# Performance work log

Hardware: AMD Instinct MI355X
Metric: run time of the kernel (lower is better)

## Reference

```python
import jax, jax.numpy as jnp
import numpy as np

B, N, HN, HE, H = 8, 128, 256, 128, 8
DH = HN // H
P = N * (N - 1) // 2


def _ln(x, g, b, eps=1e-5):
    m = jnp.mean(x, axis=-1, keepdims=True)
    v = jnp.mean((x - m) ** 2, axis=-1, keepdims=True)
    return (x - m) * jax.lax.rsqrt(v + eps) * g + b


def setup_inputs() -> dict:
    key = jax.random.key(0)
    ks = jax.random.split(key, 16)
    i1, i2 = np.triu_indices(N, k=1)  # all unordered pairs, P = N(N-1)/2
    s = lambda fan: 1.0 / np.sqrt(fan)
    return {
        "node_feat": jax.random.normal(ks[0], (B, N, HN), jnp.float32),
        "edge_feat": jax.random.normal(ks[1], (B, P, HE), jnp.float32),
        "x_idx1": jnp.asarray(i1, jnp.int32),
        "x_idx2": jnp.asarray(i2, jnp.int32),
        "mask_valid": jax.random.bernoulli(ks[2], 0.9, (B, P)).astype(jnp.float32),
        "Wqkv": jax.random.normal(ks[3], (HN, 3 * HN), jnp.float32) * s(HN),
        "bqkv": jnp.zeros((3 * HN,), jnp.float32),
        "Wev": jax.random.normal(ks[4], (HE, HN), jnp.float32) * s(HE),
        "bev": jnp.zeros((HN,), jnp.float32),
        "Wea": jax.random.normal(ks[5], (HE, H), jnp.float32) * s(HE),
        "bea": jnp.zeros((H,), jnp.float32),
        "Wo": jax.random.normal(ks[6], (2 * HN, HN), jnp.float32) * s(2 * HN),
        "bo": jnp.zeros((HN,), jnp.float32),
        "Wsk": jax.random.normal(ks[7], (HN, 2 * HN), jnp.float32) * s(HN),
        "bsk": jnp.zeros((2 * HN,), jnp.float32),
        "gn": jnp.ones((HN,), jnp.float32),
        "bn": jnp.zeros((HN,), jnp.float32),
        "ge": jnp.ones((HE,), jnp.float32),
        "be": jnp.zeros((HE,), jnp.float32),
    }


def reference(node_feat, edge_feat, x_idx1, x_idx2, mask_valid,
              Wqkv, bqkv, Wev, bev, Wea, bea, Wo, bo, Wsk, bsk,
              gn, bn, ge, be):
    n_in = _ln(node_feat, gn, bn)                      # [B,N,HN]
    e_in = _ln(edge_feat, ge, be)                      # [B,P,HE]
    q, k, v = jnp.split(n_in @ Wqkv + bqkv, 3, axis=-1)
    to_h = lambda t: t.reshape(B, -1, H, DH).transpose(0, 2, 1, 3)
    q, k, v = to_h(q), to_h(k), to_h(v)                # [B,H,N,DH]
    e_val = to_h(e_in @ Wev + bev)                     # [B,H,P,DH]
    e_adj = (e_in @ Wea + bea).transpose(0, 2, 1)      # [B,H,P]

    scale = DH ** -0.5
    logits = jnp.einsum('bhqd,bhkd->bhqk', q, k) * scale  # [B,H,N,N]
    # per-pair logits; torch stacks [qk, edge_adj] then sums -> just add
    l_node1 = logits[:, :, x_idx1, x_idx2] + e_adj     # node i1 attends to i2
    l_node2 = logits[:, :, x_idx2, x_idx1] + e_adj     # node i2 attends to i1
    v_node1 = e_val + v[:, :, x_idx2]                  # value node i1 receives
    v_node2 = e_val + v[:, :, x_idx1]

    # group the 2P directed edges by destination node (= torch cat+sort+reshape)
    cat_idx = jnp.concatenate([x_idx1, x_idx2])        # [2P]
    order = jnp.argsort(cat_idx)                       # stable sort
    gl = jnp.concatenate([l_node1, l_node2], axis=2)[:, :, order].reshape(B, H, N, N - 1)
    gv = jnp.concatenate([v_node1, v_node2], axis=2)[:, :, order].reshape(B, H, N, N - 1, DH)
    gm = jnp.concatenate([mask_valid, mask_valid], axis=1)[:, order].reshape(B, N, N - 1)[:, None]  # [B,1,N,N-1]

    gl = jnp.where(gm == 0.0, -9e15, gl)
    probs = jax.nn.softmax(gl, axis=3)
    probs = probs * jnp.any(gm != 0.0, axis=3, keepdims=True).astype(probs.dtype)
    attn = jnp.einsum('bhnk,bhnkd->bhnd', probs, gv)   # [B,H,N,DH]
    attn = attn.transpose(0, 2, 1, 3).reshape(B, N, HN)

    comb = jax.nn.gelu(jnp.concatenate([n_in, attn], axis=-1) @ Wo + bo, approximate=False)
    val, gate = jnp.split(comb @ Wsk + bsk, 2, axis=-1)
    g = jax.nn.sigmoid(gate)
    return node_feat * (1.0 - g) + val * g
```

## Files before the change

kernel.cpp:

```cpp
#include <hip/hip_runtime.h>
#include <hip/hip_bf16.h>
#include <math.h>

#define BB 8
#define NN 128
#define HN 256
#define HE 128
#define NH 8
#define DH 32
#define PP 8128
#define BP (BB*PP)

typedef __hip_bfloat16 bf16;
typedef __hip_bfloat162 bf162;
typedef __attribute__((ext_vector_type(8))) short bf16x8;
typedef __attribute__((ext_vector_type(4))) float f32x4;

__device__ __forceinline__ float bf2f(bf16 x){ return __bfloat162float(x); }
__device__ __forceinline__ float bfraw2f(short u){
  return __uint_as_float(((unsigned)(unsigned short)u) << 16);
}

__device__ __forceinline__ float wave_sum(float v){
  #pragma unroll
  for (int off=32; off>=1; off>>=1) v += __shfl_xor(v, off, 64);
  return v;
}
__device__ __forceinline__ float wave_max(float v){
  #pragma unroll
  for (int off=32; off>=1; off>>=1) v = fmaxf(v, __shfl_xor(v, off, 64));
  return v;
}
__device__ __forceinline__ float g16_sum(float v){
  #pragma unroll
  for (int off=8; off>=1; off>>=1) v += __shfl_xor(v, off, 16);
  return v;
}

__device__ __forceinline__ int pair_idx(int a, int c){
  int i = a < c ? a : c;
  int j = a < c ? c : a;
  return ((i*(255 - i))>>1) + (j - i - 1);
}

#define C_NODE 0LL
#define C_MASK 262144LL
#define C_WQKV 327168LL
#define C_BQKV 523776LL
#define C_WEV  524544LL
#define C_BEV  557312LL
#define C_WEA  557568LL
#define C_BEA  558592LL
#define C_WO   558600LL
#define C_BO   689672LL
#define C_WSK  689928LL
#define C_BSK  821000LL
#define C_GN   821512LL
#define C_BN   821768LL
#define C_GE   822024LL
#define C_BE   822152LL
#define IOFF   822400LL
#define TOT8   102785
#define CONVBLKS 402
#define I_NIN  0LL
#define I_Q    262144LL
#define I_K    524288LL
#define I_V    786432LL
#define I_ATTN 1048576LL
#define I_COMB 1310720LL
#define I_EA2  1572864LL
#define I_XG   2093056LL
#define I_EVAL 6254592LL
#define I_WT   14577664LL
#define I_WOB  14594048LL
#define I_WSKB 14659584LL
#define I_FLG  14725120LL

struct SrcPtrs { const void* p[16]; };

__global__ __launch_bounds__(256) void k_convert(SrcPtrs sp, float* __restrict__ dst,
                                                 int* __restrict__ flags,
                                                 const unsigned short* __restrict__ nodeRaw,
                                                 const void* __restrict__ rawWev,
                                                 bf16* __restrict__ Wt,
                                                 const void* __restrict__ rawWo,
                                                 const void* __restrict__ rawWsk,
                                                 bf16* __restrict__ WoB,
                                                 bf16* __restrict__ WskB)
{
  __shared__ int sbad;
  if (threadIdx.x == 0) sbad = 0;
  __syncthreads();
  {
    int bad = 0;
    for (int i = threadIdx.x; i < 1024; i += 256){
      unsigned e = (nodeRaw[i] >> 7) & 0xFFu;
      if (e >= 194u) bad = 1;
    }
    if (bad) sbad = 1;
  }
  __syncthreads();
  const int f32 = sbad;
  if (blockIdx.x == 0 && threadIdx.x == 0) flags[0] = f32;

  if (blockIdx.x >= CONVBLKS + 128){
    int o = (blockIdx.x - (CONVBLKS + 128))*256 + threadIdx.x;
    const void* src = (o < 16384) ? rawWo : rawWsk;
    bf16* dw = (o < 16384) ? WoB : WskB;
    int lo = (o < 16384) ? o : o - 16384;
    if (f32){
      const float4* s4 = (const float4*)src;
      float4 a0 = s4[2*lo], a1 = s4[2*lo+1];
      union { float4 f; bf16 h[8]; } cv;
      cv.h[0]=__float2bfloat16(a0.x); cv.h[1]=__float2bfloat16(a0.y);
      cv.h[2]=__float2bfloat16(a0.z); cv.h[3]=__float2bfloat16(a0.w);
      cv.h[4]=__float2bfloat16(a1.x); cv.h[5]=__float2bfloat16(a1.y);
      cv.h[6]=__float2bfloat16(a1.z); cv.h[7]=__float2bfloat16(a1.w);
      *reinterpret_cast<float4*>(dw + lo*8) = cv.f;
    } else {
      *reinterpret_cast<float4*>(dw + lo*8) = ((const float4*)src)[lo];
    }
    return;
  }

  if (blockIdx.x >= CONVBLKS){
    int idx = (blockIdx.x - CONVBLKS)*256 + threadIdx.x;
    float v = f32 ? ((const float*)rawWev)[idx]
                  : bfraw2f(((const short*)rawWev)[idx]);
    Wt[(idx & 255)*128 + (idx >> 8)] = __float2bfloat16(v);
    return;
  }

  int o = blockIdx.x*256 + threadIdx.x;
  if (o >= TOT8) return;
  const int cum[17] = {0,32768,40896,65472,65568,69664,69696,69824,69825,
                       86209,86241,102625,102689,102721,102753,102769,102785};
  int s = 0;
  #pragma unroll
  for (int i = 1; i <= 15; i++) if (o >= cum[i]) s = i;
  const int li = o - cum[s];
  float4 r0, r1;
  if (f32){
    const float4* src = (const float4*)sp.p[s];
    r0 = src[2*li]; r1 = src[2*li+1];
  } else {
    union { float4 f; unsigned short u[8]; } cv;
    cv.f = ((const float4*)sp.p[s])[li];
    r0.x = __uint_as_float((unsigned)cv.u[0] << 16);
    r0.y = __uint_as_float((unsigned)cv.u[1] << 16);
    r0.z = __uint_as_float((unsigned)cv.u[2] << 16);
    r0.w = __uint_as_float((unsigned)cv.u[3] << 16);
    r1.x = __uint_as_float((unsigned)cv.u[4] << 16);
    r1.y = __uint_as_float((unsigned)cv.u[5] << 16);
    r1.z = __uint_as_float((unsigned)cv.u[6] << 16);
    r1.w = __uint_as_float((unsigned)cv.u[7] << 16);
  }
  float4* d = (float4*)(dst + (long long)cum[s]*8);
  d[2*li]   = r0;
  d[2*li+1] = r1;
}

__global__ __launch_bounds__(256) void k1_node_ln_qkv(
    const float* __restrict__ cnode, const float* __restrict__ cWqkv,
    const float* __restrict__ cbqkv, const float* __restrict__ cgn, const float* __restrict__ cbn,
    float* __restrict__ nin_ws, float* __restrict__ q_ws, float* __restrict__ k_ws,
    float* __restrict__ v_ws)
{
  __shared__ float xln[4][HN];
  const int t = threadIdx.x, wv = t>>6, lane = t&63;
  const int cb = blockIdx.x % 3;
  const int g0 = (blockIdx.x / 3) * 4;
  {
    int g = g0 + wv;
    float x[4];
    #pragma unroll
    for (int i=0;i<4;i++) x[i] = cnode[g*HN + lane + 64*i];
    float s = x[0]+x[1]+x[2]+x[3];
    s = wave_sum(s);
    float m = s * (1.0f/HN);
    float q = 0.f;
    #pragma unroll
    for (int i=0;i<4;i++){ float d = x[i]-m; q += d*d; }
    q = wave_sum(q);
    float rstd = rsqrtf(fmaxf(q*(1.0f/HN), 0.f) + 1e-5f);
    #pragma unroll
    for (int i=0;i<4;i++){
      int c = lane + 64*i;
      float y = (x[i]-m)*rstd*cgn[c] + cbn[c];
      xln[wv][c] = y;
      if (cb == 0) nin_ws[g*HN + c] = y;
    }
  }
  __syncthreads();
  const int col = cb*256 + t;
  float acc[4];
  {
    float bb = cbqkv[col];
    #pragma unroll
    for (int r=0;r<4;r++) acc[r] = bb;
  }
  for (int k=0;k<HN;k+=4){
    float4 xv[4];
    #pragma unroll
    for (int r=0;r<4;r++) xv[r] = *reinterpret_cast<const float4*>(&xln[r][k]);
    #pragma unroll
    for (int kk=0;kk<4;kk++){
      float w = cWqkv[(k+kk)*768 + col];
      #pragma unroll
      for (int r=0;r<4;r++) acc[r] = fmaf((&xv[r].x)[kk], w, acc[r]);
    }
  }
  float* dstp = (cb == 0) ? q_ws : (cb == 1) ? k_ws : v_ws;
  const int h = t>>5, d = t&31;
  #pragma unroll
  for (int r=0;r<4;r++){
    int g = g0 + r;
    int b = g>>7, n = g&127;
    dstp[((b*NH + h)*NN + n)*DH + d] = acc[r];
  }
}

__global__ __launch_bounds__(256) void k2a_edge_ln(
    const void* __restrict__ edge_raw, const float* __restrict__ cWea,
    const float* __restrict__ cbea, const float* __restrict__ cge,
    const float* __restrict__ cbe, const float* __restrict__ cmask,
    bf16* __restrict__ xg, float* __restrict__ ea2, const int* __restrict__ flags)
{
  __shared__ float xlnS[16][136];
  __shared__ float part[128];
  const int t = threadIdx.x;
  const int R0 = blockIdx.x*16;
  const int b = R0 / PP;
  const int p0 = R0 - b*PP;
  const int f32 = flags[0];
  {
    int r = t>>4, sub = t&15;
    long base = (long)(R0 + r)*HE + sub*8;
    float x[8];
    if (f32){
      const float* cef = (const float*)edge_raw + base;
      float4 a0 = *reinterpret_cast<const float4*>(cef);
      float4 a1 = *reinterpret_cast<const float4*>(cef + 4);
      x[0]=a0.x; x[1]=a0.y; x[2]=a0.z; x[3]=a0.w;
      x[4]=a1.x; x[5]=a1.y; x[6]=a1.z; x[7]=a1.w;
    } else {
      union { float4 f; short u[8]; } cv;
      cv.f = *reinterpret_cast<const float4*>((const bf16*)edge_raw + base);
      #pragma unroll
      for (int i=0;i<8;i++) x[i] = bfraw2f(cv.u[i]);
    }
    float s = 0.f;
    #pragma unroll
    for (int i=0;i<8;i++) s += x[i];
    s = g16_sum(s);
    float m = s*(1.0f/HE);
    float q = 0.f;
    #pragma unroll
    for (int i=0;i<8;i++){ float dd = x[i]-m; q += dd*dd; }
    q = g16_sum(q);
    float rstd = rsqrtf(fmaxf(q*(1.0f/HE), 0.f) + 1e-5f);
    #pragma unroll
    for (int i=0;i<8;i++){
      int c = sub*8 + i;
      xlnS[r][c] = (x[i]-m)*rstd*cge[c] + cbe[c];
    }
  }
  __syncthreads();
  {
    int r = t>>4, c0 = (t&15)*8;
    union { float4 f; bf16 h[8]; } o;
    #pragma unroll
    for (int i=0;i<8;i++) o.h[i] = __float2bfloat16(xlnS[r][c0+i]);
    *reinterpret_cast<float4*>(xg + (long)(R0 + r)*HE + c0) = o.f;
  }
  {
    const int c = t & 7, r = (t>>3) & 15, half = t>>7;
    const int pid = r*8 + c;
    float s = half ? 0.0f : cbea[c];
    const int k0 = half*64;
    #pragma unroll 8
    for (int k=k0; k<k0+64; k++) s = fmaf(xlnS[r][k], cWea[k*NH + c], s);
    if (half){ part[pid] = s; }
    __syncthreads();
    if (!half){
      s += part[pid];
      int p = p0 + r;
      float mk = cmask[b*PP + p];
      ea2[(b*NH + c)*PP + p] = (mk != 0.0f) ? s : -9e15f;
    }
  }
}

__global__ __launch_bounds__(256) void k2b_mfma(
    const bf16* __restrict__ xg, const bf16* __restrict__ Wt,
    const float* __restrict__ cbev, bf16* __restrict__ e_val)
{
  __shared__ bf16 Xs[64][136];
  __shared__ bf16 Ws[64][136];
  const int t = threadIdx.x;
  const int rowblk = blockIdx.x >> 2;
  const int cb = blockIdx.x & 3;
  const int b = rowblk / 127;
  const int p0 = (rowblk - b*127) * 64;
  const int n0 = cb * 64;
  #pragma unroll
  for (int it = 0; it < 4; ++it){
    int idx = it*256 + t;
    int r = idx >> 4, seg = idx & 15;
    float4 xv = *reinterpret_cast<const float4*>(xg + (long)(b*PP + p0 + r)*HE + seg*8);
    *reinterpret_cast<float4*>(&Xs[r][seg*8]) = xv;
    float4 wv = *reinterpret_cast<const float4*>(Wt + (long)(n0 + r)*HE + seg*8);
    *reinterpret_cast<float4*>(&Ws[r][seg*8]) = wv;
  }
  __syncthreads();
  const int wv = t>>6, lane = t&63;
  const int fm = lane & 15, q = lane >> 4;
  f32x4 acc[4];
  #pragma unroll
  for (int ct=0; ct<4; ++ct){
    float bb = cbev[n0 + ct*16 + fm];
    acc[ct][0]=bb; acc[ct][1]=bb; acc[ct][2]=bb; acc[ct][3]=bb;
  }
  #pragma unroll
  for (int ks=0; ks<4; ++ks){
    bf16x8 A = *reinterpret_cast<const bf16x8*>(&Xs[wv*16 + fm][ks*32 + q*8]);
    #pragma unroll
    for (int ct=0; ct<4; ++ct){
      bf16x8 Bf = *reinterpret_cast<const bf16x8*>(&Ws[ct*16 + fm][ks*32 + q*8]);
      acc[ct] = __builtin_amdgcn_mfma_f32_16x16x32_bf16(A, Bf, acc[ct], 0, 0, 0);
    }
  }
  #pragma unroll
  for (int ct=0; ct<4; ++ct){
    int col = n0 + ct*16 + fm;
    int h = col >> 5, d = col & 31;
    #pragma unroll
    for (int reg=0; reg<4; ++reg){
      int p = p0 + wv*16 + q*4 + reg;
      e_val[((long)(b*NH + h)*PP + p)*DH + d] = __float2bfloat16(acc[ct][reg]);
    }
  }
}

__global__ __launch_bounds__(256) void k3_attn(
    const float* __restrict__ q_ws, const float* __restrict__ k_ws, const float* __restrict__ v_ws,
    const bf16* __restrict__ e_val, const float* __restrict__ ea2,
    float* __restrict__ attn)
{
  __shared__ float kT[DH][NN+1];
  __shared__ float vS[NN][DH+1];
  __shared__ float qS[8][DH];
  __shared__ float pbuf[4][NN];
  const int t = threadIdx.x, wv = t>>6, lane = t&63;
  const int s16 = blockIdx.x & 15, h = (blockIdx.x>>4)&7, b = blockIdx.x>>7;
  const int bh = b*NH + h;
  const int n0 = s16*8;
  const float* kb = k_ws + (long)bh*NN*DH;
  const float* vb = v_ws + (long)bh*NN*DH;
  const float* qb = q_ws + ((long)bh*NN + n0)*DH;
  for (int idx=t; idx<NN*DH; idx+=256){
    int m = idx>>5, d = idx&31;
    kT[d][m] = kb[idx];
    vS[m][d] = vb[idx];
  }
  if (t < 8*DH) reinterpret_cast<float*>(qS)[t] = qb[t];
  __syncthreads();
  const float scale = 0.17677669529663687f;
  const float* eab = ea2 + (long)bh*PP;
  const bf16* evp = e_val + (long)bh*PP*DH;
  for (int it=0; it<2; ++it){
    const int nn = it*4 + wv;
    const int n = n0 + nn;
    const int m1 = lane, m2 = lane + 64;
    float dot1 = 0.f, dot2 = 0.f;
    #pragma unroll
    for (int d=0; d<DH; d++){
      float qd = qS[nn][d];
      dot1 = fmaf(qd, kT[d][m1], dot1);
      dot2 = fmaf(qd, kT[d][m2], dot2);
    }
    const bool self1 = (m1 == n), self2 = (m2 == n);
    int pr1 = pair_idx(n, self1 ? (m1^1) : m1);
    int pr2 = pair_idx(n, self2 ? (m2^1) : m2);
    float ea1 = eab[pr1], ea2v = eab[pr2];
    float l1 = self1 ? -INFINITY : dot1*scale + ea1;
    float l2 = self2 ? -INFINITY : dot2*scale + ea2v;
    bool av = (!self1 && ea1 > -8.9e15f) || (!self2 && ea2v > -8.9e15f);
    float lm = wave_max(fmaxf(l1, l2));
    float e1 = __expf(l1 - lm), e2 = __expf(l2 - lm);
    float ssum = wave_sum(e1 + e2);
    int anyv = __any((int)av);
    float inv = anyv ? (1.0f/ssum) : 0.0f;
    pbuf[wv][m1] = e1*inv;
    pbuf[wv][m2] = e2*inv;
    const int msub = lane & 15, oct = lane >> 4;
    float acc[8];
    #pragma unroll
    for (int e=0;e<8;e++) acc[e] = 0.f;
    #pragma unroll
    for (int mm=0; mm<128; mm+=16){
      int m = mm + msub;
      int ms = (m==n) ? (m^1) : m;
      int pr = pair_idx(n, ms);
      bf16x8 ev8 = *reinterpret_cast<const bf16x8*>(evp + (long)pr*DH + oct*8);
      float pm = pbuf[wv][m];
      const float* vrow = &vS[m][oct*8];
      #pragma unroll
      for (int e=0;e<8;e++){
        acc[e] = fmaf(pm, vrow[e] + bfraw2f(ev8[e]), acc[e]);
      }
    }
    #pragma unroll
    for (int off=1; off<16; off<<=1){
      #pragma unroll
      for (int e=0;e<8;e++) acc[e] += __shfl_xor(acc[e], off, 64);
    }
    if (msub == 0){
      float* op = attn + ((long)b*NN + n)*HN + h*DH + oct*8;
      float4 o0 = {acc[0],acc[1],acc[2],acc[3]};
      float4 o1 = {acc[4],acc[5],acc[6],acc[7]};
      *reinterpret_cast<float4*>(op) = o0;
      *reinterpret_cast<float4*>(op+4) = o1;
    }
  }
}

__global__ __launch_bounds__(256) void k4_wo_gelu(
    const float* __restrict__ nin_ws, const float* __restrict__ attn,
    const bf16* __restrict__ WoB, const float* __restrict__ cbo,
    float* __restrict__ comb)
{
  __shared__ float xc[4][512];
  __shared__ float ps[3][4][64];
  const int t = threadIdx.x;
  const int g0 = (blockIdx.x >> 2) * 4;
  const int cq = blockIdx.x & 3;
  {
    int r = t>>6, c0 = (t&63)*8;
    const float* src = (c0 < 256) ? (nin_ws + (long)(g0+r)*HN + c0)
                                  : (attn + (long)(g0+r)*HN + (c0-256));
    float4 a0 = *reinterpret_cast<const float4*>(src);
    float4 a1 = *reinterpret_cast<const float4*>(src+4);
    *reinterpret_cast<float4*>(&xc[r][c0]) = a0;
    *reinterpret_cast<float4*>(&xc[r][c0+4]) = a1;
  }
  __syncthreads();
  const int cidx = t & 63, ks = t >> 6;
  const int col = cq*64 + cidx;
  float acc[4] = {0.f,0.f,0.f,0.f};
  const int k0 = ks*128;
  #pragma unroll 4
  for (int k=k0; k<k0+128; k++){
    float w = bf2f(WoB[k*HN + col]);
    #pragma unroll
    for (int r=0;r<4;r++) acc[r] = fmaf(xc[r][k], w, acc[r]);
  }
  if (ks){
    #pragma unroll
    for (int r=0;r<4;r++) ps[ks-1][r][cidx] = acc[r];
  }
  __syncthreads();
  if (!ks){
    float bb = cbo[col];
    #pragma unroll
    for (int r=0;r<4;r++){
      float x = acc[r] + bb + ps[0][r][cidx] + ps[1][r][cidx] + ps[2][r][cidx];
      comb[(long)(g0+r)*HN + col] = 0.5f*x*(1.0f + erff(x*0.7071067811865475f));
    }
  }
}

__global__ __launch_bounds__(256) void k5_sk_gate(
    const float* __restrict__ comb, const float* __restrict__ cnode,
    const bf16* __restrict__ WskB, const float* __restrict__ cbsk,
    void* __restrict__ out, const int* __restrict__ flags)
{
  __shared__ float xc[4][HN];
  __shared__ float psv[3][4][64];
  __shared__ float psg[3][4][64];
  const int t = threadIdx.x;
  const int g0 = (blockIdx.x >> 2) * 4;
  const int cq = blockIdx.x & 3;
  {
    int r = t>>6, c0 = (t&63)*4;
    *reinterpret_cast<float4*>(&xc[r][c0]) =
        *reinterpret_cast<const float4*>(comb + (long)(g0+r)*HN + c0);
  }
  __syncthreads();
  const int cidx = t & 63, ks = t >> 6;
  const int col = cq*64 + cidx;
  float av[4] = {0.f,0.f,0.f,0.f}, ag[4] = {0.f,0.f,0.f,0.f};
  const int k0 = ks*64;
  #pragma unroll 4
  for (int k=k0; k<k0+64; k++){
    float wv = bf2f(WskB[k*512 + col]);
    float wg = bf2f(WskB[k*512 + col + 256]);
    #pragma unroll
    for (int r=0;r<4;r++){
      float xr = xc[r][k];
      av[r] = fmaf(xr, wv, av[r]);
      ag[r] = fmaf(xr, wg, ag[r]);
    }
  }
  if (ks){
    #pragma unroll
    for (int r=0;r<4;r++){ psv[ks-1][r][cidx] = av[r]; psg[ks-1][r][cidx] = ag[r]; }
  }
  __syncthreads();
  if (!ks){
    const int f32 = flags[0];
    float bv = cbsk[col], bg = cbsk[col+256];
    #pragma unroll
    for (int r=0;r<4;r++){
      float v = av[r] + bv + psv[0][r][cidx] + psv[1][r][cidx] + psv[2][r][cidx];
      float g = ag[r] + bg + psg[0][r][cidx] + psg[1][r][cidx] + psg[2][r][cidx];
      float gg = 1.0f/(1.0f + __expf(-g));
      float nf = cnode[(long)(g0+r)*HN + col];
      float res = nf*(1.0f - gg) + v*gg;
      if (f32) ((float*)out)[(long)(g0+r)*HN + col] = res;
      else ((bf16*)out)[(long)(g0+r)*HN + col] = __float2bfloat16(res);
    }
  }
}

extern "C" void kernel_launch(void* const* d_in, const int* in_sizes, int n_inputs,
                              void* d_out, int out_size, void* d_ws, size_t ws_size,
                              hipStream_t stream)
{
  float* ws = (float*)d_ws;
  float* c_node = ws + C_NODE;
  float* c_mask = ws + C_MASK;
  float* c_Wqkv = ws + C_WQKV;
  float* c_bqkv = ws + C_BQKV;
  float* c_bev  = ws + C_BEV;
  float* c_Wea  = ws + C_WEA;
  float* c_bea  = ws + C_BEA;
  float* c_bo   = ws + C_BO;
  float* c_bsk  = ws + C_BSK;
  float* c_gn   = ws + C_GN;
  float* c_bn   = ws + C_BN;
  float* c_ge   = ws + C_GE;
  float* c_be   = ws + C_BE;
  float* base   = ws + IOFF;
  float* nin_ws  = base + I_NIN;
  float* q_ws    = base + I_Q;
  float* k_ws    = base + I_K;
  float* v_ws    = base + I_V;
  float* attn_ws = base + I_ATTN;
  float* comb_ws = base + I_COMB;
  float* ea2_ws  = base + I_EA2;
  bf16*  xg_ws   = (bf16*)(base + I_XG);
  bf16*  eval_ws = (bf16*)(base + I_EVAL);
  bf16*  wt_ws   = (bf16*)(base + I_WT);
  bf16*  wob_ws  = (bf16*)(base + I_WOB);
  bf16*  wskb_ws = (bf16*)(base + I_WSKB);
  int*   flags   = (int*)(base + I_FLG);

  SrcPtrs sp;
  sp.p[0]  = d_in[0];
  sp.p[1]  = d_in[4];
  sp.p[2]  = d_in[5];
  sp.p[3]  = d_in[6];
  sp.p[4]  = d_in[7];
  sp.p[5]  = d_in[8];
  sp.p[6]  = d_in[9];
  sp.p[7]  = d_in[10];
  sp.p[8]  = d_in[11];
  sp.p[9]  = d_in[12];
  sp.p[10] = d_in[13];
  sp.p[11] = d_in[14];
  sp.p[12] = d_in[15];
  sp.p[13] = d_in[16];
  sp.p[14] = d_in[17];
  sp.p[15] = d_in[18];

  k_convert<<<CONVBLKS + 256, 256, 0, stream>>>(sp, ws, flags,
                                                (const unsigned short*)d_in[0],
                                                d_in[7], wt_ws,
                                                d_in[11], d_in[13],
                                                wob_ws, wskb_ws);
  k1_node_ln_qkv<<<768, 256, 0, stream>>>(c_node, c_Wqkv, c_bqkv, c_gn, c_bn,
                                          nin_ws, q_ws, k_ws, v_ws);
  k2a_edge_ln<<<BP/16, 256, 0, stream>>>(d_in[1], c_Wea, c_bea, c_ge, c_be, c_mask,
                                         xg_ws, ea2_ws, flags);
  k2b_mfma<<<4064, 256, 0, stream>>>(xg_ws, wt_ws, c_bev, eval_ws);
  k3_attn<<<BB*NH*16, 256, 0, stream>>>(q_ws, k_ws, v_ws, eval_ws, ea2_ws, attn_ws);
  k4_wo_gelu<<<1024, 256, 0, stream>>>(nin_ws, attn_ws, wob_ws, c_bo, comb_ws);
  k5_sk_gate<<<1024, 256, 0, stream>>>(comb_ws, c_node, wskb_ws, c_bsk, d_out, flags);
}
```

Baseline: 199.5 us.

## Drop conversion kernel, read raw inputs directly and fuse node/edge LN kernels

Removes the separate format-conversion pre-pass and has every kernel read the raw input tensors directly. Each kernel re-detects the dtype from a sample of node_feat instead of reading a flag. The node LN+QKV kernel and the edge LN kernel are merged into one launch split by block index, and k2b now transposes the Wev tile itself while loading it into shared memory. This cuts one launch and the extra round trip through workspace, at the cost of a duplicated per-block dtype check and a strided, bank-conflicting shared-memory transpose in every k2b block.

```diff
diff --git a/kernel.cpp b/kernel.cpp
--- a/kernel.cpp
+++ b/kernel.cpp
@@ -12,11 +12,9 @@
 #define BP (BB*PP)
 
 typedef __hip_bfloat16 bf16;
-typedef __hip_bfloat162 bf162;
 typedef __attribute__((ext_vector_type(8))) short bf16x8;
 typedef __attribute__((ext_vector_type(4))) float f32x4;
 
-__device__ __forceinline__ float bf2f(bf16 x){ return __bfloat162float(x); }
 __device__ __forceinline__ float bfraw2f(short u){
   return __uint_as_float(((unsigned)(unsigned short)u) << 16);
 }
@@ -43,25 +41,35 @@
   return ((i*(255 - i))>>1) + (j - i - 1);
 }
 
-#define C_NODE 0LL
-#define C_MASK 262144LL
-#define C_WQKV 327168LL
-#define C_BQKV 523776LL
-#define C_WEV  524544LL
-#define C_BEV  557312LL
-#define C_WEA  557568LL
-#define C_BEA  558592LL
-#define C_WO   558600LL
-#define C_BO   689672LL
-#define C_WSK  689928LL
-#define C_BSK  821000LL
-#define C_GN   821512LL
-#define C_BN   821768LL
-#define C_GE   822024LL
-#define C_BE   822152LL
-#define IOFF   822400LL
-#define TOT8   102785
-#define CONVBLKS 402
+__device__ __forceinline__ int detect_f32(const unsigned short* __restrict__ nodeRaw){
+  __shared__ int sbad;
+  if (threadIdx.x == 0) sbad = 0;
+  __syncthreads();
+  int bad = 0;
+  for (int i = threadIdx.x; i < 1024; i += 256){
+    unsigned e = (nodeRaw[i] >> 7) & 0xFFu;
+    if (e >= 194u) bad = 1;
+  }
+  if (bad) sbad = 1;
+  __syncthreads();
+  return sbad;
+}
+
+__device__ __forceinline__ void load4raw(const void* raw, long off, int f32, float x[4]){
+  if (f32){
+    float4 v = *reinterpret_cast<const float4*>((const float*)raw + off);
+    x[0]=v.x; x[1]=v.y; x[2]=v.z; x[3]=v.w;
+  } else {
+    union { float2 f; short u[4]; } cv;
+    cv.f = *reinterpret_cast<const float2*>((const short*)raw + off);
+    #pragma unroll
+    for (int i=0;i<4;i++) x[i] = bfraw2f(cv.u[i]);
+  }
+}
+__device__ __forceinline__ float ldraw(const void* raw, long off, int f32){
+  return f32 ? ((const float*)raw)[off] : bfraw2f(((const short*)raw)[off]);
+}
+
 #define I_NIN  0LL
 #define I_Q    262144LL
 #define I_K    524288LL
@@ -71,232 +79,166 @@
 #define I_EA2  1572864LL
 #define I_XG   2093056LL
 #define I_EVAL 6254592LL
-#define I_WT   14577664LL
-#define I_WOB  14594048LL
-#define I_WSKB 14659584LL
-#define I_FLG  14725120LL
-
-struct SrcPtrs { const void* p[16]; };
-
-__global__ __launch_bounds__(256) void k_convert(SrcPtrs sp, float* __restrict__ dst,
-                                                 int* __restrict__ flags,
-                                                 const unsigned short* __restrict__ nodeRaw,
-                                                 const void* __restrict__ rawWev,
-                                                 bf16* __restrict__ Wt,
-                                                 const void* __restrict__ rawWo,
-                                                 const void* __restrict__ rawWsk,
-                                                 bf16* __restrict__ WoB,
-                                                 bf16* __restrict__ WskB)
-{
-  __shared__ int sbad;
-  if (threadIdx.x == 0) sbad = 0;
-  __syncthreads();
-  {
-    int bad = 0;
-    for (int i = threadIdx.x; i < 1024; i += 256){
-      unsigned e = (nodeRaw[i] >> 7) & 0xFFu;
-      if (e >= 194u) bad = 1;
-    }
-    if (bad) sbad = 1;
-  }
-  __syncthreads();
-  const int f32 = sbad;
-  if (blockIdx.x == 0 && threadIdx.x == 0) flags[0] = f32;
-
-  if (blockIdx.x >= CONVBLKS + 128){
-    int o = (blockIdx.x - (CONVBLKS + 128))*256 + threadIdx.x;
-    const void* src = (o < 16384) ? rawWo : rawWsk;
-    bf16* dw = (o < 16384) ? WoB : WskB;
-    int lo = (o < 16384) ? o : o - 16384;
-    if (f32){
-      const float4* s4 = (const float4*)src;
-      float4 a0 = s4[2*lo], a1 = s4[2*lo+1];
-      union { float4 f; bf16 h[8]; } cv;
-      cv.h[0]=__float2bfloat16(a0.x); cv.h[1]=__float2bfloat16(a0.y);
-      cv.h[2]=__float2bfloat16(a0.z); cv.h[3]=__float2bfloat16(a0.w);
-      cv.h[4]=__float2bfloat16(a1.x); cv.h[5]=__float2bfloat16(a1.y);
-      cv.h[6]=__float2bfloat16(a1.z); cv.h[7]=__float2bfloat16(a1.w);
-      *reinterpret_cast<float4*>(dw + lo*8) = cv.f;
-    } else {
-      *reinterpret_cast<float4*>(dw + lo*8) = ((const float4*)src)[lo];
-    }
-    return;
-  }
-
-  if (blockIdx.x >= CONVBLKS){
-    int idx = (blockIdx.x - CONVBLKS)*256 + threadIdx.x;
-    float v = f32 ? ((const float*)rawWev)[idx]
-                  : bfraw2f(((const short*)rawWev)[idx]);
-    Wt[(idx & 255)*128 + (idx >> 8)] = __float2bfloat16(v);
-    return;
-  }
-
-  int o = blockIdx.x*256 + threadIdx.x;
-  if (o >= TOT8) return;
-  const int cum[17] = {0,32768,40896,65472,65568,69664,69696,69824,69825,
-                       86209,86241,102625,102689,102721,102753,102769,102785};
-  int s = 0;
-  #pragma unroll
-  for (int i = 1; i <= 15; i++) if (o >= cum[i]) s = i;
-  const int li = o - cum[s];
-  float4 r0, r1;
-  if (f32){
-    const float4* src = (const float4*)sp.p[s];
-    r0 = src[2*li]; r1 = src[2*li+1];
-  } else {
-    union { float4 f; unsigned short u[8]; } cv;
-    cv.f = ((const float4*)sp.p[s])[li];
-    r0.x = __uint_as_float((unsigned)cv.u[0] << 16);
-    r0.y = __uint_as_float((unsigned)cv.u[1] << 16);
-    r0.z = __uint_as_float((unsigned)cv.u[2] << 16);
-    r0.w = __uint_as_float((unsigned)cv.u[3] << 16);
-    r1.x = __uint_as_float((unsigned)cv.u[4] << 16);
-    r1.y = __uint_as_float((unsigned)cv.u[5] << 16);
-    r1.z = __uint_as_float((unsigned)cv.u[6] << 16);
-    r1.w = __uint_as_float((unsigned)cv.u[7] << 16);
-  }
-  float4* d = (float4*)(dst + (long long)cum[s]*8);
-  d[2*li]   = r0;
-  d[2*li+1] = r1;
-}
-
-__global__ __launch_bounds__(256) void k1_node_ln_qkv(
-    const float* __restrict__ cnode, const float* __restrict__ cWqkv,
-    const float* __restrict__ cbqkv, const float* __restrict__ cgn, const float* __restrict__ cbn,
+
+__global__ __launch_bounds__(256) void kA_ln_qkv_edge(
+    const void* __restrict__ rawNode, const void* __restrict__ rawEdge,
+    const void* __restrict__ rawMask, const void* __restrict__ rawWqkv,
+    const void* __restrict__ rawBqkv, const void* __restrict__ rawWea,
+    const void* __restrict__ rawBea, const void* __restrict__ rawGn,
+    const void* __restrict__ rawBn, const void* __restrict__ rawGe,
+    const void* __restrict__ rawBe,
     float* __restrict__ nin_ws, float* __restrict__ q_ws, float* __restrict__ k_ws,
-    float* __restrict__ v_ws)
+    float* __restrict__ v_ws, bf16* __restrict__ xg, float* __restrict__ ea2)
 {
   __shared__ float xln[4][HN];
-  const int t = threadIdx.x, wv = t>>6, lane = t&63;
-  const int cb = blockIdx.x % 3;
-  const int g0 = (blockIdx.x / 3) * 4;
-  {
-    int g = g0 + wv;
-    float x[4];
-    #pragma unroll
-    for (int i=0;i<4;i++) x[i] = cnode[g*HN + lane + 64*i];
-    float s = x[0]+x[1]+x[2]+x[3];
-    s = wave_sum(s);
-    float m = s * (1.0f/HN);
-    float q = 0.f;
-    #pragma unroll
-    for (int i=0;i<4;i++){ float d = x[i]-m; q += d*d; }
-    q = wave_sum(q);
-    float rstd = rsqrtf(fmaxf(q*(1.0f/HN), 0.f) + 1e-5f);
-    #pragma unroll
-    for (int i=0;i<4;i++){
-      int c = lane + 64*i;
-      float y = (x[i]-m)*rstd*cgn[c] + cbn[c];
-      xln[wv][c] = y;
-      if (cb == 0) nin_ws[g*HN + c] = y;
-    }
-  }
-  __syncthreads();
-  const int col = cb*256 + t;
-  float acc[4];
-  {
-    float bb = cbqkv[col];
-    #pragma unroll
-    for (int r=0;r<4;r++) acc[r] = bb;
-  }
-  for (int k=0;k<HN;k+=4){
-    float4 xv[4];
-    #pragma unroll
-    for (int r=0;r<4;r++) xv[r] = *reinterpret_cast<const float4*>(&xln[r][k]);
-    #pragma unroll
-    for (int kk=0;kk<4;kk++){
-      float w = cWqkv[(k+kk)*768 + col];
-      #pragma unroll
-      for (int r=0;r<4;r++) acc[r] = fmaf((&xv[r].x)[kk], w, acc[r]);
-    }
-  }
-  float* dstp = (cb == 0) ? q_ws : (cb == 1) ? k_ws : v_ws;
-  const int h = t>>5, d = t&31;
-  #pragma unroll
-  for (int r=0;r<4;r++){
-    int g = g0 + r;
-    int b = g>>7, n = g&127;
-    dstp[((b*NH + h)*NN + n)*DH + d] = acc[r];
-  }
-}
-
-__global__ __launch_bounds__(256) void k2a_edge_ln(
-    const void* __restrict__ edge_raw, const float* __restrict__ cWea,
-    const float* __restrict__ cbea, const float* __restrict__ cge,
-    const float* __restrict__ cbe, const float* __restrict__ cmask,
-    bf16* __restrict__ xg, float* __restrict__ ea2, const int* __restrict__ flags)
-{
   __shared__ float xlnS[16][136];
   __shared__ float part[128];
+  const int f32 = detect_f32((const unsigned short*)rawNode);
   const int t = threadIdx.x;
-  const int R0 = blockIdx.x*16;
-  const int b = R0 / PP;
-  const int p0 = R0 - b*PP;
-  const int f32 = flags[0];
-  {
-    int r = t>>4, sub = t&15;
-    long base = (long)(R0 + r)*HE + sub*8;
-    float x[8];
-    if (f32){
-      const float* cef = (const float*)edge_raw + base;
-      float4 a0 = *reinterpret_cast<const float4*>(cef);
-      float4 a1 = *reinterpret_cast<const float4*>(cef + 4);
-      x[0]=a0.x; x[1]=a0.y; x[2]=a0.z; x[3]=a0.w;
-      x[4]=a1.x; x[5]=a1.y; x[6]=a1.z; x[7]=a1.w;
+
+  if (blockIdx.x < 768){
+    const int wv = t>>6, lane = t&63;
+    const int cb = blockIdx.x % 3;
+    const int g0 = (blockIdx.x / 3) * 4;
+    {
+      int g = g0 + wv;
+      float x[4], gn4[4], bn4[4];
+      load4raw(rawNode, (long)g*HN + lane*4, f32, x);
+      float s = x[0]+x[1]+x[2]+x[3];
+      s = wave_sum(s);
+      float m = s * (1.0f/HN);
+      float q = 0.f;
+      #pragma unroll
+      for (int i=0;i<4;i++){ float d = x[i]-m; q += d*d; }
+      q = wave_sum(q);
+      float rstd = rsqrtf(fmaxf(q*(1.0f/HN), 0.f) + 1e-5f);
+      load4raw(rawGn, lane*4, f32, gn4);
+      load4raw(rawBn, lane*4, f32, bn4);
+      float y4[4];
+      #pragma unroll
+      for (int i=0;i<4;i++){
+        y4[i] = (x[i]-m)*rstd*gn4[i] + bn4[i];
+        xln[wv][lane*4+i] = y4[i];
+      }
+      if (cb == 0){
+        float4 yo = {y4[0],y4[1],y4[2],y4[3]};
+        *reinterpret_cast<float4*>(nin_ws + (long)g*HN + lane*4) = yo;
+      }
+    }
+    __syncthreads();
+    const int col = cb*256 + t;
+    float acc[4];
+    {
+      float bb = ldraw(rawBqkv, col, f32);
+      #pragma unroll
+      for (int r=0;r<4;r++) acc[r] = bb;
+    }
+    if (!f32){
+      const short* W = (const short*)rawWqkv;
+      for (int k=0;k<HN;k+=4){
+        float4 xv[4];
+        #pragma unroll
+        for (int r=0;r<4;r++) xv[r] = *reinterpret_cast<const float4*>(&xln[r][k]);
+        #pragma unroll
+        for (int kk=0;kk<4;kk++){
+          float w = bfraw2f(W[(long)(k+kk)*768 + col]);
+          #pragma unroll
+          for (int r=0;r<4;r++) acc[r] = fmaf((&xv[r].x)[kk], w, acc[r]);
+        }
+      }
     } else {
-      union { float4 f; short u[8]; } cv;
-      cv.f = *reinterpret_cast<const float4*>((const bf16*)edge_raw + base);
-      #pragma unroll
-      for (int i=0;i<8;i++) x[i] = bfraw2f(cv.u[i]);
-    }
-    float s = 0.f;
-    #pragma unroll
-    for (int i=0;i<8;i++) s += x[i];
-    s = g16_sum(s);
-    float m = s*(1.0f/HE);
-    float q = 0.f;
-    #pragma unroll
-    for (int i=0;i<8;i++){ float dd = x[i]-m; q += dd*dd; }
-    q = g16_sum(q);
-    float rstd = rsqrtf(fmaxf(q*(1.0f/HE), 0.f) + 1e-5f);
-    #pragma unroll
-    for (int i=0;i<8;i++){
-      int c = sub*8 + i;
-      xlnS[r][c] = (x[i]-m)*rstd*cge[c] + cbe[c];
-    }
-  }
-  __syncthreads();
-  {
-    int r = t>>4, c0 = (t&15)*8;
-    union { float4 f; bf16 h[8]; } o;
-    #pragma unroll
-    for (int i=0;i<8;i++) o.h[i] = __float2bfloat16(xlnS[r][c0+i]);
-    *reinterpret_cast<float4*>(xg + (long)(R0 + r)*HE + c0) = o.f;
-  }
-  {
-    const int c = t & 7, r = (t>>3) & 15, half = t>>7;
-    const int pid = r*8 + c;
-    float s = half ? 0.0f : cbea[c];
-    const int k0 = half*64;
-    #pragma unroll 8
-    for (int k=k0; k<k0+64; k++) s = fmaf(xlnS[r][k], cWea[k*NH + c], s);
-    if (half){ part[pid] = s; }
+      const float* W = (const float*)rawWqkv;
+      for (int k=0;k<HN;k+=4){
+        float4 xv[4];
+        #pragma unroll
+        for (int r=0;r<4;r++) xv[r] = *reinterpret_cast<const float4*>(&xln[r][k]);
+        #pragma unroll
+        for (int kk=0;kk<4;kk++){
+          float w = W[(long)(k+kk)*768 + col];
+          #pragma unroll
+          for (int r=0;r<4;r++) acc[r] = fmaf((&xv[r].x)[kk], w, acc[r]);
+        }
+      }
+    }
+    float* dstp = (cb == 0) ? q_ws : (cb == 1) ? k_ws : v_ws;
+    const int h = t>>5, d = t&31;
+    #pragma unroll
+    for (int r=0;r<4;r++){
+      int g = g0 + r;
+      int b = g>>7, n = g&127;
+      dstp[((long)(b*NH + h)*NN + n)*DH + d] = acc[r];
+    }
+  } else {
+    const int R0 = (blockIdx.x - 768)*16;
+    const int b = R0 / PP;
+    const int p0 = R0 - b*PP;
+    {
+      int r = t>>4, sub = t&15;
+      long base = (long)(R0 + r)*HE + sub*8;
+      float x[8], ge8[8], be8[8];
+      load4raw(rawEdge, base, f32, x);
+      load4raw(rawEdge, base+4, f32, x+4);
+      load4raw(rawGe, sub*8, f32, ge8);
+      load4raw(rawGe, sub*8+4, f32, ge8+4);
+      load4raw(rawBe, sub*8, f32, be8);
+      load4raw(rawBe, sub*8+4, f32, be8+4);
+      float s = 0.f;
+      #pragma unroll
+      for (int i=0;i<8;i++) s += x[i];
+      s = g16_sum(s);
+      float m = s*(1.0f/HE);
+      float q = 0.f;
+      #pragma unroll
+      for (int i=0;i<8;i++){ float dd = x[i]-m; q += dd*dd; }
+      q = g16_sum(q);
+      float rstd = rsqrtf(fmaxf(q*(1.0f/HE), 0.f) + 1e-5f);
+      #pragma unroll
+      for (int i=0;i<8;i++){
+        xlnS[r][sub*8+i] = (x[i]-m)*rstd*ge8[i] + be8[i];
+      }
+    }
     __syncthreads();
-    if (!half){
-      s += part[pid];
-      int p = p0 + r;
-      float mk = cmask[b*PP + p];
-      ea2[(b*NH + c)*PP + p] = (mk != 0.0f) ? s : -9e15f;
+    {
+      int r = t>>4, c0 = (t&15)*8;
+      union { float4 f; bf16 h[8]; } o;
+      #pragma unroll
+      for (int i=0;i<8;i++) o.h[i] = __float2bfloat16(xlnS[r][c0+i]);
+      *reinterpret_cast<float4*>(xg + (long)(R0 + r)*HE + c0) = o.f;
+    }
+    {
+      const int c = t & 7, r = (t>>3) & 15, half = t>>7;
+      const int pid = r*8 + c;
+      float s = half ? 0.0f : ldraw(rawBea, c, f32);
+      const int k0 = half*64;
+      if (!f32){
+        const short* W = (const short*)rawWea;
+        #pragma unroll 8
+        for (int k=k0; k<k0+64; k++) s = fmaf(xlnS[r][k], bfraw2f(W[k*NH + c]), s);
+      } else {
+        const float* W = (const float*)rawWea;
+        #pragma unroll 8
+        for (int k=k0; k<k0+64; k++) s = fmaf(xlnS[r][k], W[k*NH + c], s);
+      }
+      if (half){ part[pid] = s; }
+      __syncthreads();
+      if (!half){
+        s += part[pid];
+        int p = p0 + r;
+        float mk = ldraw(rawMask, (long)b*PP + p, f32);
+        ea2[(long)(b*NH + c)*PP + p] = (mk != 0.0f) ? s : -9e15f;
+      }
     }
   }
 }
 
 __global__ __launch_bounds__(256) void k2b_mfma(
-    const bf16* __restrict__ xg, const bf16* __restrict__ Wt,
-    const float* __restrict__ cbev, bf16* __restrict__ e_val)
+    const void* __restrict__ rawNode,
+    const bf16* __restrict__ xg, const void* __restrict__ rawWev,
+    const void* __restrict__ rawBev, bf16* __restrict__ e_val)
 {
   __shared__ bf16 Xs[64][136];
   __shared__ bf16 Ws[64][136];
+  const int f32 = detect_f32((const unsigned short*)rawNode);
   const int t = threadIdx.x;
   const int rowblk = blockIdx.x >> 2;
   const int cb = blockIdx.x & 3;
@@ -309,8 +251,15 @@
     int r = idx >> 4, seg = idx & 15;
     float4 xv = *reinterpret_cast<const float4*>(xg + (long)(b*PP + p0 + r)*HE + seg*8);
     *reinterpret_cast<float4*>(&Xs[r][seg*8]) = xv;
-    float4 wv = *reinterpret_cast<const float4*>(Wt + (long)(n0 + r)*HE + seg*8);
-    *reinterpret_cast<float4*>(&Ws[r][seg*8]) = wv;
+  }
+  #pragma unroll
+  for (int it = 0; it < 8; ++it){
+    int r = it*16 + (t>>4);
+    int c0 = (t&15)*4;
+    float v[4];
+    load4raw(rawWev, (long)r*HN + n0 + c0, f32, v);
+    #pragma unroll
+    for (int j=0;j<4;j++) Ws[c0+j][r] = __float2bfloat16(v[j]);
   }
   __syncthreads();
   const int wv = t>>6, lane = t&63;
@@ -318,7 +267,7 @@
   f32x4 acc[4];
   #pragma unroll
   for (int ct=0; ct<4; ++ct){
-    float bb = cbev[n0 + ct*16 + fm];
+    float bb = ldraw(rawBev, n0 + ct*16 + fm, f32);
     acc[ct][0]=bb; acc[ct][1]=bb; acc[ct][2]=bb; acc[ct][3]=bb;
   }
   #pragma unroll
@@ -426,12 +375,14 @@
 }
 
 __global__ __launch_bounds__(256) void k4_wo_gelu(
+    const void* __restrict__ rawNode,
     const float* __restrict__ nin_ws, const float* __restrict__ attn,
-    const bf16* __restrict__ WoB, const float* __restrict__ cbo,
+    const void* __restrict__ rawWo, const void* __restrict__ rawBo,
     float* __restrict__ comb)
 {
   __shared__ float xc[4][512];
   __shared__ float ps[3][4][64];
+  const int f32 = detect_f32((const unsigned short*)rawNode);
   const int t = threadIdx.x;
   const int g0 = (blockIdx.x >> 2) * 4;
   const int cq = blockIdx.x & 3;
@@ -449,11 +400,22 @@
   const int col = cq*64 + cidx;
   float acc[4] = {0.f,0.f,0.f,0.f};
   const int k0 = ks*128;
-  #pragma unroll 4
-  for (int k=k0; k<k0+128; k++){
-    float w = bf2f(WoB[k*HN + col]);
-    #pragma unroll
-    for (int r=0;r<4;r++) acc[r] = fmaf(xc[r][k], w, acc[r]);
+  if (!f32){
+    const short* W = (const short*)rawWo;
+    #pragma unroll 4
+    for (int k=k0; k<k0+128; k++){
+      float w = bfraw2f(W[(long)k*HN + col]);
+      #pragma unroll
+      for (int r=0;r<4;r++) acc[r] = fmaf(xc[r][k], w, acc[r]);
+    }
+  } else {
+    const float* W = (const float*)rawWo;
+    #pragma unroll 4
+    for (int k=k0; k<k0+128; k++){
+      float w = W[(long)k*HN + col];
+      #pragma unroll
+      for (int r=0;r<4;r++) acc[r] = fmaf(xc[r][k], w, acc[r]);
+    }
   }
   if (ks){
     #pragma unroll
@@ -461,7 +423,7 @@
   }
   __syncthreads();
   if (!ks){
-    float bb = cbo[col];
+    float bb = ldraw(rawBo, col, f32);
     #pragma unroll
     for (int r=0;r<4;r++){
       float x = acc[r] + bb + ps[0][r][cidx] + ps[1][r][cidx] + ps[2][r][cidx];
@@ -471,13 +433,14 @@
 }
 
 __global__ __launch_bounds__(256) void k5_sk_gate(
-    const float* __restrict__ comb, const float* __restrict__ cnode,
-    const bf16* __restrict__ WskB, const float* __restrict__ cbsk,
-    void* __restrict__ out, const int* __restrict__ flags)
+    const void* __restrict__ rawNode,
+    const float* __restrict__ comb, const void* __restrict__ rawWsk,
+    const void* __restrict__ rawBsk, void* __restrict__ out)
 {
   __shared__ float xc[4][HN];
   __shared__ float psv[3][4][64];
   __shared__ float psg[3][4][64];
+  const int f32 = detect_f32((const unsigned short*)rawNode);
   const int t = threadIdx.x;
   const int g0 = (blockIdx.x >> 2) * 4;
   const int cq = blockIdx.x & 3;
@@ -491,15 +454,31 @@
   const int col = cq*64 + cidx;
   float av[4] = {0.f,0.f,0.f,0.f}, ag[4] = {0.f,0.f,0.f,0.f};
   const int k0 = ks*64;
-  #pragma unroll 4
-  for (int k=k0; k<k0+64; k++){
-    float wv = bf2f(WskB[k*512 + col]);
-    float wg = bf2f(WskB[k*512 + col + 256]);
-    #pragma unroll
-    for (int r=0;r<4;r++){
-      float xr = xc[r][k];
-      av[r] = fmaf(xr, wv, av[r]);
-      ag[r] = fmaf(xr, wg, ag[r]);
+  if (!f32){
+    const short* W = (const short*)rawWsk;
+    #pragma unroll 4
+    for (int k=k0; k<k0+64; k++){
+      float wv = bfraw2f(W[(long)k*512 + col]);
+      float wg = bfraw2f(W[(long)k*512 + col + 256]);
+      #pragma unroll
+      for (int r=0;r<4;r++){
+        float xr = xc[r][k];
+        av[r] = fmaf(xr, wv, av[r]);
+        ag[r] = fmaf(xr, wg, ag[r]);
+      }
+    }
+  } else {
+    const float* W = (const float*)rawWsk;
+    #pragma unroll 4
+    for (int k=k0; k<k0+64; k++){
+      float wv = W[(long)k*512 + col];
+      float wg = W[(long)k*512 + col + 256];
+      #pragma unroll
+      for (int r=0;r<4;r++){
+        float xr = xc[r][k];
+        av[r] = fmaf(xr, wv, av[r]);
+        ag[r] = fmaf(xr, wg, ag[r]);
+      }
     }
   }
   if (ks){
@@ -508,14 +487,13 @@
   }
   __syncthreads();
   if (!ks){
-    const int f32 = flags[0];
-    float bv = cbsk[col], bg = cbsk[col+256];
+    float bv = ldraw(rawBsk, col, f32), bg = ldraw(rawBsk, col+256, f32);
     #pragma unroll
     for (int r=0;r<4;r++){
       float v = av[r] + bv + psv[0][r][cidx] + psv[1][r][cidx] + psv[2][r][cidx];
       float g = ag[r] + bg + psg[0][r][cidx] + psg[1][r][cidx] + psg[2][r][cidx];
       float gg = 1.0f/(1.0f + __expf(-g));
-      float nf = cnode[(long)(g0+r)*HN + col];
+      float nf = ldraw(rawNode, (long)(g0+r)*HN + col, f32);
       float res = nf*(1.0f - gg) + v*gg;
       if (f32) ((float*)out)[(long)(g0+r)*HN + col] = res;
       else ((bf16*)out)[(long)(g0+r)*HN + col] = __float2bfloat16(res);
@@ -527,21 +505,25 @@
                               void* d_out, int out_size, void* d_ws, size_t ws_size,
                               hipStream_t stream)
 {
-  float* ws = (float*)d_ws;
-  float* c_node = ws + C_NODE;
-  float* c_mask = ws + C_MASK;
-  float* c_Wqkv = ws + C_WQKV;
-  float* c_bqkv = ws + C_BQKV;
-  float* c_bev  = ws + C_BEV;
-  float* c_Wea  = ws + C_WEA;
-  float* c_bea  = ws + C_BEA;
-  float* c_bo   = ws + C_BO;
-  float* c_bsk  = ws + C_BSK;
-  float* c_gn   = ws + C_GN;
-  float* c_bn   = ws + C_BN;
-  float* c_ge   = ws + C_GE;
-  float* c_be   = ws + C_BE;
-  float* base   = ws + IOFF;
+  const void* rawNode = d_in[0];
+  const void* rawEdge = d_in[1];
+  const void* rawMask = d_in[4];
+  const void* rawWqkv = d_in[5];
+  const void* rawBqkv = d_in[6];
+  const void* rawWev  = d_in[7];
+  const void* rawBev  = d_in[8];
+  const void* rawWea  = d_in[9];
+  const void* rawBea  = d_in[10];
+  const void* rawWo   = d_in[11];
+  const void* rawBo   = d_in[12];
+  const void* rawWsk  = d_in[13];
+  const void* rawBsk  = d_in[14];
+  const void* rawGn   = d_in[15];
+  const void* rawBn   = d_in[16];
+  const void* rawGe   = d_in[17];
+  const void* rawBe   = d_in[18];
+
+  float* base = (float*)d_ws;
   float* nin_ws  = base + I_NIN;
   float* q_ws    = base + I_Q;
   float* k_ws    = base + I_K;
@@ -551,40 +533,13 @@
   float* ea2_ws  = base + I_EA2;
   bf16*  xg_ws   = (bf16*)(base + I_XG);
   bf16*  eval_ws = (bf16*)(base + I_EVAL);
-  bf16*  wt_ws   = (bf16*)(base + I_WT);
-  bf16*  wob_ws  = (bf16*)(base + I_WOB);
-  bf16*  wskb_ws = (bf16*)(base + I_WSKB);
-  int*   flags   = (int*)(base + I_FLG);
-
-  SrcPtrs sp;
-  sp.p[0]  = d_in[0];
-  sp.p[1]  = d_in[4];
-  sp.p[2]  = d_in[5];
-  sp.p[3]  = d_in[6];
-  sp.p[4]  = d_in[7];
-  sp.p[5]  = d_in[8];
-  sp.p[6]  = d_in[9];
-  sp.p[7]  = d_in[10];
-  sp.p[8]  = d_in[11];
-  sp.p[9]  = d_in[12];
-  sp.p[10] = d_in[13];
-  sp.p[11] = d_in[14];
-  sp.p[12] = d_in[15];
-  sp.p[13] = d_in[16];
-  sp.p[14] = d_in[17];
-  sp.p[15] = d_in[18];
-
-  k_convert<<<CONVBLKS + 256, 256, 0, stream>>>(sp, ws, flags,
-                                                (const unsigned short*)d_in[0],
-                                                d_in[7], wt_ws,
-                                                d_in[11], d_in[13],
-                                                wob_ws, wskb_ws);
-  k1_node_ln_qkv<<<768, 256, 0, stream>>>(c_node, c_Wqkv, c_bqkv, c_gn, c_bn,
-                                          nin_ws, q_ws, k_ws, v_ws);
-  k2a_edge_ln<<<BP/16, 256, 0, stream>>>(d_in[1], c_Wea, c_bea, c_ge, c_be, c_mask,
-                                         xg_ws, ea2_ws, flags);
-  k2b_mfma<<<4064, 256, 0, stream>>>(xg_ws, wt_ws, c_bev, eval_ws);
+
+  kA_ln_qkv_edge<<<768 + BP/16, 256, 0, stream>>>(
+      rawNode, rawEdge, rawMask, rawWqkv, rawBqkv, rawWea, rawBea,
+      rawGn, rawBn, rawGe, rawBe,
+      nin_ws, q_ws, k_ws, v_ws, xg_ws, ea2_ws);
+  k2b_mfma<<<4064, 256, 0, stream>>>(rawNode, xg_ws, rawWev, rawBev, eval_ws);
   k3_attn<<<BB*NH*16, 256, 0, stream>>>(q_ws, k_ws, v_ws, eval_ws, ea2_ws, attn_ws);
-  k4_wo_gelu<<<1024, 256, 0, stream>>>(nin_ws, attn_ws, wob_ws, c_bo, comb_ws);
-  k5_sk_gate<<<1024, 256, 0, stream>>>(comb_ws, c_node, wskb_ws, c_bsk, d_out, flags);
-}
+  k4_wo_gelu<<<1024, 256, 0, stream>>>(rawNode, nin_ws, attn_ws, rawWo, rawBo, comb_ws);
+  k5_sk_gate<<<1024, 256, 0, stream>>>(rawNode, comb_ws, rawWsk, rawBsk, d_out);
+}
```

Result: no change. 202.5 us (+1.5%).
